# Kernel optimization log

Hardware: AMD Instinct MI355X
Metric: run time of the kernel (lower is better)

The kernel has to match this reference:

```python
import jax, jax.numpy as jnp
import numpy as np

NUM_HEADS = 8
NUM_LEVELS = 4
NUM_POINTS = 8
EMBED = 256
SPATIAL_SHAPES = ((92, 160), (46, 80), (23, 40), (12, 20))


def _bilinear_sample(vl, gx, gy, H, W):
    # vl: [N, d, H*W]; gx, gy: [N, Q, P], grid coords in [-1, 1]
    # matches F.grid_sample(mode='bilinear', padding_mode='zeros', align_corners=False)
    x = (gx + 1.0) * (W * 0.5) - 0.5
    y = (gy + 1.0) * (H * 0.5) - 0.5
    x0 = jnp.floor(x)
    y0 = jnp.floor(y)
    wx = x - x0
    wy = y - y0
    x0i = x0.astype(jnp.int32)
    y0i = y0.astype(jnp.int32)
    N, Q, P = gx.shape
    d = vl.shape[1]

    def gather(xi, yi):
        valid = ((xi >= 0) & (xi < W) & (yi >= 0) & (yi < H)).astype(vl.dtype)
        idx = jnp.clip(yi, 0, H - 1) * W + jnp.clip(xi, 0, W - 1)  # [N, Q, P]
        flat = jnp.broadcast_to(idx.reshape(N, 1, Q * P), (N, d, Q * P))
        got = jnp.take_along_axis(vl, flat, axis=2).reshape(N, d, Q, P)
        return got * valid[:, None]

    return (gather(x0i, y0i) * ((1 - wx) * (1 - wy))[:, None]
            + gather(x0i + 1, y0i) * (wx * (1 - wy))[:, None]
            + gather(x0i, y0i + 1) * ((1 - wx) * wy)[:, None]
            + gather(x0i + 1, y0i + 1) * (wx * wy)[:, None])


def _forward(query, value, reference_points, spatial_shapes,
             W_off, b_off, W_attn, b_attn, W_val, b_val, W_out, b_out):
    shapes = np.asarray(spatial_shapes)  # static per-level (H, W)
    bs, Q, C = query.shape
    H, Lv, P = NUM_HEADS, NUM_LEVELS, NUM_POINTS
    d = C // H
    # value projection, split into heads: [bs*H, d, Ltot]
    v = value @ W_val + b_val
    v = v.reshape(bs, -1, H, d).transpose(0, 2, 3, 1).reshape(bs * H, d, -1)
    # sampling offsets [bs, Q, H, Lv, P, 2]
    off = (query @ W_off + b_off).reshape(bs, Q, H, Lv, P, 2)
    # attention weights, softmax over Lv*P
    aw = jax.nn.softmax((query @ W_attn + b_attn).reshape(bs, Q, H, Lv * P), axis=-1)
    aw = aw.reshape(bs, Q, H, Lv, P).transpose(0, 2, 1, 3, 4).reshape(bs * H, Q, Lv, P)
    # normalize offsets by level (W, H)
    norm = jnp.asarray([[w_, h_] for h_, w_ in shapes], dtype=query.dtype)  # [Lv, 2]
    loc = reference_points[:, :, None, :, None, :] + off / norm[None, None, None, :, None, :]
    grids = (2.0 * loc - 1.0).transpose(0, 2, 1, 3, 4, 5).reshape(bs * H, Q, Lv, P, 2)
    out = jnp.zeros((bs * H, d, Q), dtype=query.dtype)
    start = 0
    for lvl in range(Lv):
        H_l, W_l = int(shapes[lvl, 0]), int(shapes[lvl, 1])
        vl = v[:, :, start:start + H_l * W_l]
        g = grids[:, :, lvl]  # [bs*H, Q, P, 2]
        s = _bilinear_sample(vl, g[..., 0], g[..., 1], H_l, W_l)  # [bs*H, d, Q, P]
        out = out + jnp.einsum('ndqp,nqp->ndq', s, aw[:, :, lvl])
        start += H_l * W_l
    out = out.reshape(bs, H, d, Q).transpose(0, 3, 1, 2).reshape(bs, Q, C)
    return out @ W_out + b_out


def setup_inputs() -> dict:
    key = jax.random.key(0)
    ks = jax.random.split(key, 9)
    bs, Q = 6, 4096  # 6 cameras x (64x64 BEV queries)
    Ltot = sum(h * w for h, w in SPATIAL_SHAPES)  # 19560
    HLP2 = NUM_HEADS * NUM_LEVELS * NUM_POINTS * 2  # 512
    HLP = NUM_HEADS * NUM_LEVELS * NUM_POINTS  # 256
    s = 0.02
    return {
        "query": jax.random.normal(ks[0], (bs, Q, EMBED), jnp.float32),
        "value": jax.random.normal(ks[1], (bs, Ltot, EMBED), jnp.float32),
        "reference_points": jax.random.uniform(ks[2], (bs, Q, NUM_LEVELS, 2), jnp.float32),
        "spatial_shapes": jnp.asarray(SPATIAL_SHAPES, jnp.int32),
        "W_off": s * jax.random.normal(ks[3], (EMBED, HLP2), jnp.float32),
        "b_off": s * jax.random.normal(ks[4], (HLP2,), jnp.float32),
        "W_attn": s * jax.random.normal(ks[5], (EMBED, HLP), jnp.float32),
        "b_attn": s * jax.random.normal(ks[6], (HLP,), jnp.float32),
        "W_val": s * jax.random.normal(ks[7], (EMBED, EMBED), jnp.float32),
        "b_val": jnp.zeros((EMBED,), jnp.float32),
        "W_out": s * jax.random.normal(ks[8], (EMBED, EMBED), jnp.float32),
        "b_out": jnp.zeros((EMBED,), jnp.float32),
    }


def reference(query, value, reference_points, spatial_shapes,
              W_off, b_off, W_attn, b_attn, W_val, b_val, W_out, b_out):
    return _forward(query, value, reference_points, spatial_shapes,
                    W_off, b_off, W_attn, b_attn, W_val, b_val, W_out, b_out)
```

## Files before the change

kernel.cpp:

```cpp
#include <hip/hip_runtime.h>
#include <hip/hip_fp16.h>
#include <stdint.h>

#define BS 6
#define NQ 4096
#define NH 8
#define EMB 256
#define LTOT 19560
#define ROWS_V 117360
#define ROWS_VP 117376
#define ROWS_Q 24576
#define VBLK 917
#define QBLK 1152

typedef __attribute__((ext_vector_type(8))) short bf16x8;
typedef __attribute__((ext_vector_type(4))) float floatx4;
typedef __attribute__((ext_vector_type(8))) unsigned short ushort8v;

__device__ __forceinline__ ushort f2bf(float f) {
    union { float f; uint32_t i; } c; c.f = f;
    uint32_t r = c.i + 0x7FFFu + ((c.i >> 16) & 1u);
    return (ushort)(r >> 16);
}
__device__ __forceinline__ ushort f2h(float f) {
    __half h = __float2half(f);
    union { __half h; ushort u; } c; c.h = h; return c.u;
}
__device__ __forceinline__ float h2f(ushort u) {
    union { ushort u; __half h; } c; c.u = u; return __half2float(c.h);
}

__device__ __forceinline__ void gll16(const ushort* g, ushort* l) {
    __builtin_amdgcn_global_load_lds(
        (const __attribute__((address_space(1))) void*)g,
        (__attribute__((address_space(3))) void*)l, 16, 0, 0);
}

template<int L>
__device__ __forceinline__ float bcastf(float x) {
    return __int_as_float(
        __builtin_amdgcn_ds_swizzle(__float_as_int(x), 0x1C | (L << 5)));
}
template<int L>
__device__ __forceinline__ uint32_t bcastu(uint32_t x) {
    return (uint32_t)__builtin_amdgcn_ds_swizzle((int)x, 0x1C | (L << 5));
}

__device__ __forceinline__ void fmx_lo(float& acc, float w, uint32_t u) {
    asm("v_fma_mix_f32 %0, %1, %2, %0 op_sel:[0,0,0] op_sel_hi:[0,1,0]"
        : "+v"(acc) : "v"(w), "v"(u));
}
__device__ __forceinline__ void fmx_hi(float& acc, float w, uint32_t u) {
    asm("v_fma_mix_f32 %0, %1, %2, %0 op_sel:[0,1,0] op_sel_hi:[0,1,0]"
        : "+v"(acc) : "v"(w), "v"(u));
}

__global__ __launch_bounds__(256) void prep(
    const float* __restrict__ W_val, const float* __restrict__ W_off,
    const float* __restrict__ W_attn, const float* __restrict__ W_out,
    const float* __restrict__ b_off, const float* __restrict__ b_attn,
    ushort* __restrict__ Wvt, ushort* __restrict__ Wq,
    ushort* __restrict__ Wot, float* __restrict__ bcat)
{
    int id = blockIdx.x * 256 + threadIdx.x;
    if (id < 65536) {
        int n = id >> 8, k = id & 255;
        Wvt[id] = f2bf(W_val[k * 256 + n]);
        return;
    }
    id -= 65536;
    if (id < 131072) {
        int n = id >> 8, k = id & 255;
        Wq[id] = f2bf(W_off[k * 512 + n]);
        return;
    }
    id -= 131072;
    if (id < 65536) {
        int n = id >> 8, k = id & 255;
        Wq[131072 + id] = f2bf(W_attn[k * 256 + n]);
        return;
    }
    id -= 65536;
    if (id < 65536) {
        int n = id >> 8, k = id & 255;
        Wot[id] = f2bf(W_out[k * 256 + n]);
        return;
    }
    id -= 65536;
    if (id < 768) bcat[id] = (id < 512) ? b_off[id] : b_attn[id - 512];
}

__global__ __launch_bounds__(512) void front(
    const float* __restrict__ value,
    const float* __restrict__ query,
    const ushort* __restrict__ Wvt,
    const ushort* __restrict__ Wq,
    const float* __restrict__ b_val,
    const float* __restrict__ bcat,
    ushort* __restrict__ v_out,
    ushort* __restrict__ qp_out)
{
    constexpr int K = 256;
    __shared__ ushort As[128 * 32];
    __shared__ ushort Bs[256 * 32];

    const int t = threadIdx.x;
    const int w = t >> 6;
    const int lane = t & 63;
    const int bid = blockIdx.x;

    if (bid < VBLK) {
        constexpr int N = 256, M = ROWS_V;
        const int bm = bid * 128;
        const int wm = (w >> 2) * 64;
        const int wn = (w & 3) * 64;

        const int arow = t >> 2;
        const int acol = (t & 3) * 8;
        const bool rowok = (bm + arow) < M;
        const float* Ap = value + (size_t)(bm + arow) * K + acol;
        ushort* Asw = &As[arow * 32 + acol];

        const int srow = lane >> 2;
        const int scol = (lane & 3) * 8;
        const ushort* Bg0 = Wvt + (size_t)(w * 32 + srow) * K + scol;
        const ushort* Bg1 = Wvt + (size_t)(w * 32 + 16 + srow) * K + scol;
        ushort* Bl0 = &Bs[(w * 32) * 32];
        ushort* Bl1 = &Bs[(w * 32 + 16) * 32];

        const ushort* apt = &As[(wm + (lane & 15)) * 32 + (lane >> 4) * 8];
        const ushort* bpt = &Bs[(wn + (lane & 15)) * 32 + (lane >> 4) * 8];

        floatx4 acc[4][4] = {};

        for (int kt = 0; kt < K; kt += 32) {
            float4 f0, f1;
            if (rowok) {
                f0 = *(const float4*)(Ap + kt);
                f1 = *(const float4*)(Ap + kt + 4);
            } else {
                f0 = make_float4(0.f, 0.f, 0.f, 0.f);
                f1 = f0;
            }
            __syncthreads();
            gll16(Bg0 + kt, Bl0);
            gll16(Bg1 + kt, Bl1);
            ushort8v u;
            u[0] = f2bf(f0.x); u[1] = f2bf(f0.y); u[2] = f2bf(f0.z); u[3] = f2bf(f0.w);
            u[4] = f2bf(f1.x); u[5] = f2bf(f1.y); u[6] = f2bf(f1.z); u[7] = f2bf(f1.w);
            *(ushort8v*)Asw = u;
            __syncthreads();

            bf16x8 a[4], b[4];
            #pragma unroll
            for (int i = 0; i < 4; ++i) {
                a[i] = *(const bf16x8*)(apt + i * 16 * 32);
                b[i] = *(const bf16x8*)(bpt + i * 16 * 32);
            }
            #pragma unroll
            for (int i = 0; i < 4; ++i)
                #pragma unroll
                for (int j = 0; j < 4; ++j)
                    acc[i][j] = __builtin_amdgcn_mfma_f32_16x16x32_bf16(
                        a[i], b[j], acc[i][j], 0, 0, 0);
        }

        const int crow = (lane >> 4) * 4;
        const int ccol = lane & 15;
        #pragma unroll
        for (int j = 0; j < 4; ++j) {
            int gcol = wn + j * 16 + ccol;
            float bv = b_val[gcol];
            #pragma unroll
            for (int i = 0; i < 4; ++i) {
                #pragma unroll
                for (int r = 0; r < 4; ++r) {
                    int grow = bm + wm + i * 16 + crow + r;
                    if (grow < M)
                        v_out[(size_t)grow * N + gcol] = f2h(acc[i][j][r] + bv);
                }
            }
        }
    } else {
        constexpr int N = 768;
        const int qbid = bid - VBLK;
        const int bm = (qbid % 192) * 128;
        const int bn = (qbid / 192) * 128;
        const int wm = (w >> 1) * 32;
        const int wn = (w & 1) * 64;

        const int arow = t >> 2;
        const int acol = (t & 3) * 8;
        const float* Ap = query + (size_t)(bm + arow) * K + acol;
        ushort* Asw = &As[arow * 32 + acol];

        const int srow = lane >> 2;
        const int scol = (lane & 3) * 8;
        const ushort* Bg0 = Wq + (size_t)(bn + w * 16 + srow) * K + scol;
        ushort* Bl0 = &Bs[(w * 16) * 32];

        const ushort* apt = &As[(wm + (lane & 15)) * 32 + (lane >> 4) * 8];
        const ushort* bpt = &Bs[(wn + (lane & 15)) * 32 + (lane >> 4) * 8];

        floatx4 acc[2][4] = {};

        for (int kt = 0; kt < K; kt += 32) {
            float4 f0 = *(const float4*)(Ap + kt);
            float4 f1 = *(const float4*)(Ap + kt + 4);
            __syncthreads();
            gll16(Bg0 + kt, Bl0);
            ushort8v u;
            u[0] = f2bf(f0.x); u[1] = f2bf(f0.y); u[2] = f2bf(f0.z); u[3] = f2bf(f0.w);
            u[4] = f2bf(f1.x); u[5] = f2bf(f1.y); u[6] = f2bf(f1.z); u[7] = f2bf(f1.w);
            *(ushort8v*)Asw = u;
            __syncthreads();

            bf16x8 a[2], b[4];
            #pragma unroll
            for (int i = 0; i < 2; ++i)
                a[i] = *(const bf16x8*)(apt + i * 16 * 32);
            #pragma unroll
            for (int j = 0; j < 4; ++j)
                b[j] = *(const bf16x8*)(bpt + j * 16 * 32);
            #pragma unroll
            for (int i = 0; i < 2; ++i)
                #pragma unroll
                for (int j = 0; j < 4; ++j)
                    acc[i][j] = __builtin_amdgcn_mfma_f32_16x16x32_bf16(
                        a[i], b[j], acc[i][j], 0, 0, 0);
        }

        const int crow = (lane >> 4) * 4;
        const int ccol = lane & 15;
        #pragma unroll
        for (int j = 0; j < 4; ++j) {
            int gcol = bn + wn + j * 16 + ccol;
            float bv = bcat[gcol];
            #pragma unroll
            for (int i = 0; i < 2; ++i) {
                int grow = bm + wm + i * 16 + crow;
                #pragma unroll
                for (int r = 0; r < 4; ++r)
                    qp_out[(size_t)(grow + r) * N + gcol] = f2h(acc[i][j][r] + bv);
            }
        }
    }
}

__global__ __launch_bounds__(256) void gemm_bt(
    const ushort* __restrict__ A,
    const ushort* __restrict__ Bt,
    const float* __restrict__ bias,
    float* __restrict__ C, int M, int N)
{
    constexpr int K = 256;
    __shared__ ushort As[128 * 32];
    __shared__ ushort Bs[128 * 32];

    const int t = threadIdx.x;
    const int w = t >> 6;
    const int lane = t & 63;
    const int bm = blockIdx.x * 128;
    const int bn = blockIdx.y * 128;
    const int wm = (w >> 1) * 64;
    const int wn = (w & 1) * 64;

    floatx4 acc[4][4] = {};

    const int srow = lane >> 2;
    const int scol = (lane & 3) * 8;
    const ushort* Ag0 = A + (size_t)(bm + (w * 2 + 0) * 16 + srow) * K + scol;
    const ushort* Ag1 = A + (size_t)(bm + (w * 2 + 1) * 16 + srow) * K + scol;
    const ushort* Bg0 = Bt + (size_t)(bn + (w * 2 + 0) * 16 + srow) * K + scol;
    const ushort* Bg1 = Bt + (size_t)(bn + (w * 2 + 1) * 16 + srow) * K + scol;
    ushort* Al0 = &As[(w * 2 + 0) * 512];
    ushort* Al1 = &As[(w * 2 + 1) * 512];
    ushort* Bl0 = &Bs[(w * 2 + 0) * 512];
    ushort* Bl1 = &Bs[(w * 2 + 1) * 512];

    const ushort* apt = &As[(wm + (lane & 15)) * 32 + (lane >> 4) * 8];
    const ushort* bpt = &Bs[(wn + (lane & 15)) * 32 + (lane >> 4) * 8];

    for (int kt = 0; kt < K; kt += 32) {
        __syncthreads();
        gll16(Ag0 + kt, Al0);
        gll16(Ag1 + kt, Al1);
        gll16(Bg0 + kt, Bl0);
        gll16(Bg1 + kt, Bl1);
        __syncthreads();

        bf16x8 a[4], b[4];
        #pragma unroll
        for (int i = 0; i < 4; ++i) {
            a[i] = *(const bf16x8*)(apt + i * 16 * 32);
            b[i] = *(const bf16x8*)(bpt + i * 16 * 32);
        }
        #pragma unroll
        for (int i = 0; i < 4; ++i)
            #pragma unroll
            for (int j = 0; j < 4; ++j)
                acc[i][j] = __builtin_amdgcn_mfma_f32_16x16x32_bf16(
                    a[i], b[j], acc[i][j], 0, 0, 0);
    }

    const int crow = (lane >> 4) * 4;
    const int ccol = lane & 15;
    #pragma unroll
    for (int j = 0; j < 4; ++j) {
        int gcol = bn + wn + j * 16 + ccol;
        float bv = bias[gcol];
        #pragma unroll
        for (int i = 0; i < 4; ++i) {
            #pragma unroll
            for (int r = 0; r < 4; ++r) {
                int grow = bm + wm + i * 16 + crow + r;
                if (grow < M)
                    C[(size_t)grow * N + gcol] = acc[i][j][r] + bv;
            }
        }
    }
}

__global__ __launch_bounds__(256) void sampler4(
    const ushort* __restrict__ v,
    const ushort* __restrict__ qp,
    const float* __restrict__ ref,
    ushort* __restrict__ agg)
{
    __shared__ char ballast[49152];
    if (blockIdx.x > 0x7FFFFFF0u) {
        ballast[threadIdx.x] = (char)threadIdx.x;
        agg[0] = (ushort)ballast[(threadIdx.x * 37) & 4095];
    }

    const int bid = (blockIdx.x & 7) * 384 + (blockIdx.x >> 3);

    const int tid = threadIdx.x;
    const int g = bid * 64 + (tid >> 2);
    const int st = tid & 3;
    const int h = g & 7;
    const int bq = g >> 3;
    const int b = bid >> 9;

    const int Wl = 160 >> st;
    const int Hl = (st == 3) ? 12 : (92 >> st);
    const int Sl = (st == 0) ? 0 : (st == 1) ? 14720 : (st == 2) ? 18400 : 19320;

    const ushort* qrow = qp + (size_t)bq * 768;

    float px[8], py[8];
    {
        ushort8v uo0 = *(const ushort8v*)(qrow + h * 64 + st * 16);
        ushort8v uo1 = *(const ushort8v*)(qrow + h * 64 + st * 16 + 8);
        float2 rf = *(const float2*)(ref + (size_t)bq * 8 + st * 2);
        const float fW = (float)Wl, fH = (float)Hl;
        #pragma unroll
        for (int i = 0; i < 4; ++i) {
            px[i]     = fmaf(rf.x, fW, h2f(uo0[2 * i]))     - 0.5f;
            py[i]     = fmaf(rf.y, fH, h2f(uo0[2 * i + 1])) - 0.5f;
            px[i + 4] = fmaf(rf.x, fW, h2f(uo1[2 * i]))     - 0.5f;
            py[i + 4] = fmaf(rf.y, fH, h2f(uo1[2 * i + 1])) - 0.5f;
        }
    }

    float a8[8];
    {
        ushort8v ul = *(const ushort8v*)(qrow + 512 + h * 32 + st * 8);
        #pragma unroll
        for (int i = 0; i < 8; ++i) a8[i] = h2f(ul[i]);
        float m = a8[0];
        #pragma unroll
        for (int i = 1; i < 8; ++i) m = fmaxf(m, a8[i]);
        m = fmaxf(m, __shfl_xor(m, 1, 4));
        m = fmaxf(m, __shfl_xor(m, 2, 4));
        float s = 0.f;
        #pragma unroll
        for (int i = 0; i < 8; ++i) { a8[i] = __expf(a8[i] - m); s += a8[i]; }
        s += __shfl_xor(s, 1, 4);
        s += __shfl_xor(s, 2, 4);
        float inv = 1.f / s;
        #pragma unroll
        for (int i = 0; i < 8; ++i) a8[i] *= inv;
    }

    const char* vb = (const char*)(v + (size_t)b * (LTOT * EMB));
    const uint32_t coffB = (uint32_t)(h * 64 + st * 16);

    float acc[8] = {0.f, 0.f, 0.f, 0.f, 0.f, 0.f, 0.f, 0.f};

    #pragma unroll
    for (int idx = 0; idx < 8; ++idx) {
        float px_ = px[idx], py_ = py[idx];
        float x0f = floorf(px_), y0f = floorf(py_);
        float wx = px_ - x0f, wy = py_ - y0f;
        int x0 = (int)x0f, y0 = (int)y0f;
        int x1 = x0 + 1, y1 = y0 + 1;
        float vx0 = ((uint32_t)x0 < (uint32_t)Wl) ? 1.f : 0.f;
        float vx1 = ((uint32_t)x1 < (uint32_t)Wl) ? 1.f : 0.f;
        float vy0 = ((uint32_t)y0 < (uint32_t)Hl) ? 1.f : 0.f;
        float vy1 = ((uint32_t)y1 < (uint32_t)Hl) ? 1.f : 0.f;
        int cx0 = min(max(x0, 0), Wl - 1);
        int cx1 = min(max(x1, 0), Wl - 1);
        int cy0 = min(max(y0, 0), Hl - 1);
        int cy1 = min(max(y1, 0), Hl - 1);
        float aw = a8[idx];
        float omx = 1.f - wx, omy = 1.f - wy;
        float omya = omy * aw, wya = wy * aw;
        float w00 = omx * omya * (vx0 * vy0);
        float w10 = wx  * omya * (vx1 * vy0);
        float w01 = omx * wya  * (vx0 * vy1);
        float w11 = wx  * wya  * (vx1 * vy1);
        int r0 = Sl + cy0 * Wl;
        int r1 = Sl + cy1 * Wl;
        uint32_t e00 = (uint32_t)(r0 + cx0) << 9;
        uint32_t e10 = (uint32_t)(r0 + cx1) << 9;
        uint32_t e01 = (uint32_t)(r1 + cx0) << 9;
        uint32_t e11 = (uint32_t)(r1 + cx1) << 9;

        #define ACCMIX(w_, c_) \
            fmx_lo(acc[0], w_, c_.x); fmx_hi(acc[1], w_, c_.x); \
            fmx_lo(acc[2], w_, c_.y); fmx_hi(acc[3], w_, c_.y); \
            fmx_lo(acc[4], w_, c_.z); fmx_hi(acc[5], w_, c_.z); \
            fmx_lo(acc[6], w_, c_.w); fmx_hi(acc[7], w_, c_.w);
        #define DO_LEVEL(L) { \
            float W00 = bcastf<L>(w00), W10 = bcastf<L>(w10); \
            float W01 = bcastf<L>(w01), W11 = bcastf<L>(w11); \
            uint32_t E00 = bcastu<L>(e00), E10 = bcastu<L>(e10); \
            uint32_t E01 = bcastu<L>(e01), E11 = bcastu<L>(e11); \
            uint4 c00 = *(const uint4*)(vb + (E00 + coffB)); \
            uint4 c10 = *(const uint4*)(vb + (E10 + coffB)); \
            uint4 c01 = *(const uint4*)(vb + (E01 + coffB)); \
            uint4 c11 = *(const uint4*)(vb + (E11 + coffB)); \
            ACCMIX(W00, c00); ACCMIX(W10, c10); \
            ACCMIX(W01, c01); ACCMIX(W11, c11); }
        DO_LEVEL(0)
        DO_LEVEL(1)
        DO_LEVEL(2)
        DO_LEVEL(3)
        #undef DO_LEVEL
        #undef ACCMIX
    }

    ushort8v r;
    #pragma unroll
    for (int i = 0; i < 8; ++i) r[i] = f2bf(acc[i]);
    *(ushort8v*)(agg + (size_t)bq * 256 + h * 32 + st * 8) = r;
}

extern "C" void kernel_launch(void* const* d_in, const int* in_sizes, int n_in,
                              void* d_out, int out_size, void* d_ws, size_t ws_size,
                              hipStream_t stream) {
    const float* query  = (const float*)d_in[0];
    const float* value  = (const float*)d_in[1];
    const float* refpts = (const float*)d_in[2];
    const float* W_off  = (const float*)d_in[4];
    const float* b_off  = (const float*)d_in[5];
    const float* W_attn = (const float*)d_in[6];
    const float* b_attn = (const float*)d_in[7];
    const float* W_val  = (const float*)d_in[8];
    const float* b_val  = (const float*)d_in[9];
    const float* W_out  = (const float*)d_in[10];
    const float* b_out  = (const float*)d_in[11];
    float* out = (float*)d_out;

    char* ws = (char*)d_ws;
    ushort* v_bf   = (ushort*)(ws);
    ushort* qp     = (ushort*)(ws + 72679424ull);
    ushort* agg_bf = (ushort*)(ws + 148176896ull);
    ushort* Wvt    = (ushort*)(ws + 160759808ull);
    ushort* Wq     = (ushort*)(ws + 160890880ull);
    ushort* Wot    = (ushort*)(ws + 161284096ull);
    float*  bcat   = (float*) (ws + 161415168ull);

    prep<<<1283, 256, 0, stream>>>(W_val, W_off, W_attn, W_out,
                                   b_off, b_attn, Wvt, Wq, Wot, bcat);

    front<<<VBLK + QBLK, 512, 0, stream>>>(
        value, query, Wvt, Wq, b_val, bcat, v_bf, qp);

    sampler4<<<(ROWS_Q * NH) / 64, 256, 0, stream>>>(
        v_bf, qp, refpts, agg_bf);

    gemm_bt<<<dim3(ROWS_Q / 128, 2), 256, 0, stream>>>(
        agg_bf, Wot, b_out, out, ROWS_Q, 256);
}
```

Before: 404.8 us.

## Restructure front GEMM: resident swizzled B tile in LDS, A streamed to registers

```diff
diff --git a/kernel.cpp b/kernel.cpp
--- a/kernel.cpp
+++ b/kernel.cpp
@@ -10,8 +10,8 @@
 #define ROWS_V 117360
 #define ROWS_VP 117376
 #define ROWS_Q 24576
-#define VBLK 917
-#define QBLK 1152
+#define VB2 1834
+#define QB 1152
 
 typedef __attribute__((ext_vector_type(8))) short bf16x8;
 typedef __attribute__((ext_vector_type(4))) float floatx4;
@@ -28,6 +28,11 @@
 }
 __device__ __forceinline__ float h2f(ushort u) {
     union { ushort u; __half h; } c; c.u = u; return __half2float(c.h);
+}
+__device__ __forceinline__ uint32_t cvtpk(float a, float b) {
+    uint32_t r;
+    asm("v_cvt_pk_bf16_f32 %0, %1, %2" : "=v"(r) : "v"(a), "v"(b));
+    return r;
 }
 
 __device__ __forceinline__ void gll16(const ushort* g, ushort* l) {
@@ -65,19 +70,19 @@
     int id = blockIdx.x * 256 + threadIdx.x;
     if (id < 65536) {
         int n = id >> 8, k = id & 255;
-        Wvt[id] = f2bf(W_val[k * 256 + n]);
+        Wvt[id ^ ((n & 7) << 3)] = f2bf(W_val[k * 256 + n]);
         return;
     }
     id -= 65536;
     if (id < 131072) {
         int n = id >> 8, k = id & 255;
-        Wq[id] = f2bf(W_off[k * 512 + n]);
+        Wq[id ^ ((n & 7) << 3)] = f2bf(W_off[k * 512 + n]);
         return;
     }
     id -= 131072;
     if (id < 65536) {
         int n = id >> 8, k = id & 255;
-        Wq[131072 + id] = f2bf(W_attn[k * 256 + n]);
+        Wq[131072 + (id ^ ((n & 7) << 3))] = f2bf(W_attn[k * 256 + n]);
         return;
     }
     id -= 65536;
@@ -90,7 +95,7 @@
     if (id < 768) bcat[id] = (id < 512) ? b_off[id] : b_attn[id - 512];
 }
 
-__global__ __launch_bounds__(512) void front(
+__global__ __launch_bounds__(512, 4) void front(
     const float* __restrict__ value,
     const float* __restrict__ query,
     const ushort* __restrict__ Wvt,
@@ -100,148 +105,101 @@
     ushort* __restrict__ v_out,
     ushort* __restrict__ qp_out)
 {
-    constexpr int K = 256;
-    __shared__ ushort As[128 * 32];
-    __shared__ ushort Bs[256 * 32];
+    __shared__ ushort Bs[128 * 256];
 
     const int t = threadIdx.x;
     const int w = t >> 6;
     const int lane = t & 63;
     const int bid = blockIdx.x;
 
-    if (bid < VBLK) {
-        constexpr int N = 256, M = ROWS_V;
-        const int bm = bid * 128;
-        const int wm = (w >> 2) * 64;
-        const int wn = (w & 3) * 64;
-
-        const int arow = t >> 2;
-        const int acol = (t & 3) * 8;
-        const bool rowok = (bm + arow) < M;
-        const float* Ap = value + (size_t)(bm + arow) * K + acol;
-        ushort* Asw = &As[arow * 32 + acol];
-
-        const int srow = lane >> 2;
-        const int scol = (lane & 3) * 8;
-        const ushort* Bg0 = Wvt + (size_t)(w * 32 + srow) * K + scol;
-        const ushort* Bg1 = Wvt + (size_t)(w * 32 + 16 + srow) * K + scol;
-        ushort* Bl0 = &Bs[(w * 32) * 32];
-        ushort* Bl1 = &Bs[(w * 32 + 16) * 32];
-
-        const ushort* apt = &As[(wm + (lane & 15)) * 32 + (lane >> 4) * 8];
-        const ushort* bpt = &Bs[(wn + (lane & 15)) * 32 + (lane >> 4) * 8];
-
-        floatx4 acc[4][4] = {};
-
-        for (int kt = 0; kt < K; kt += 32) {
+    const float* Ap;
+    const ushort* Bsrc;
+    const float* bias;
+    ushort* Cout;
+    int Nout, bm, bn, Mrows;
+    if (bid < VB2) {
+        int m = bid >> 1, nh = bid & 1;
+        bm = m * 128; bn = nh * 128;
+        Ap = value; Bsrc = Wvt + bn * 256; bias = b_val; Cout = v_out;
+        Nout = 256; Mrows = ROWS_V;
+    } else {
+        int qb = bid - VB2;
+        int m = qb / 6, nh = qb - m * 6;
+        bm = m * 128; bn = nh * 128;
+        Ap = query; Bsrc = Wq + bn * 256; bias = bcat; Cout = qp_out;
+        Nout = 768; Mrows = ROWS_Q;
+    }
+
+    #pragma unroll
+    for (int i = 0; i < 8; ++i)
+        gll16(Bsrc + i * 4096 + t * 8, &Bs[i * 4096 + t * 8]);
+    __syncthreads();
+
+    const int wm = (w >> 2) * 64;
+    const int wn = (w & 3) * 32;
+    const int ks = (lane >> 4) * 8;
+    const int arow0 = bm + wm + (lane & 15);
+
+    const int nl0 = wn + (lane & 15);
+    const int bsw = (nl0 & 7) << 3;
+    int bbase[2];
+    #pragma unroll
+    for (int j = 0; j < 2; ++j)
+        bbase[j] = (nl0 + j * 16) * 256 + ks;
+
+    const float* arow_p[4];
+    bool rok[4];
+    #pragma unroll
+    for (int i = 0; i < 4; ++i) {
+        int r = arow0 + i * 16;
+        rok[i] = r < Mrows;
+        arow_p[i] = Ap + (size_t)r * 256 + ks;
+    }
+
+    floatx4 acc[4][2] = {};
+
+    for (int kt = 0; kt < 256; kt += 32) {
+        bf16x8 a[4], b[2];
+        #pragma unroll
+        for (int i = 0; i < 4; ++i) {
             float4 f0, f1;
-            if (rowok) {
-                f0 = *(const float4*)(Ap + kt);
-                f1 = *(const float4*)(Ap + kt + 4);
+            if (rok[i]) {
+                f0 = *(const float4*)(arow_p[i] + kt);
+                f1 = *(const float4*)(arow_p[i] + kt + 4);
             } else {
-                f0 = make_float4(0.f, 0.f, 0.f, 0.f);
-                f1 = f0;
+                f0 = make_float4(0.f, 0.f, 0.f, 0.f); f1 = f0;
             }
-            __syncthreads();
-            gll16(Bg0 + kt, Bl0);
-            gll16(Bg1 + kt, Bl1);
-            ushort8v u;
-            u[0] = f2bf(f0.x); u[1] = f2bf(f0.y); u[2] = f2bf(f0.z); u[3] = f2bf(f0.w);
-            u[4] = f2bf(f1.x); u[5] = f2bf(f1.y); u[6] = f2bf(f1.z); u[7] = f2bf(f1.w);
-            *(ushort8v*)Asw = u;
-            __syncthreads();
-
-            bf16x8 a[4], b[4];
+            union { uint32_t u[4]; bf16x8 v; } cc;
+            cc.u[0] = cvtpk(f0.x, f0.y);
+            cc.u[1] = cvtpk(f0.z, f0.w);
+            cc.u[2] = cvtpk(f1.x, f1.y);
+            cc.u[3] = cvtpk(f1.z, f1.w);
+            a[i] = cc.v;
+        }
+        #pragma unroll
+        for (int j = 0; j < 2; ++j)
+            b[j] = *(const bf16x8*)&Bs[(bbase[j] + kt) ^ bsw];
+        #pragma unroll
+        for (int i = 0; i < 4; ++i)
             #pragma unroll
-            for (int i = 0; i < 4; ++i) {
-                a[i] = *(const bf16x8*)(apt + i * 16 * 32);
-                b[i] = *(const bf16x8*)(bpt + i * 16 * 32);
-            }
+            for (int j = 0; j < 2; ++j)
+                acc[i][j] = __builtin_amdgcn_mfma_f32_16x16x32_bf16(
+                    a[i], b[j], acc[i][j], 0, 0, 0);
+    }
+
+    const int crow = (lane >> 4) * 4;
+    const int ccol = lane & 15;
+    #pragma unroll
+    for (int j = 0; j < 2; ++j) {
+        int gcol = bn + wn + j * 16 + ccol;
+        float bv = bias[gcol];
+        #pragma unroll
+        for (int i = 0; i < 4; ++i) {
             #pragma unroll
-            for (int i = 0; i < 4; ++i)
-                #pragma unroll
-                for (int j = 0; j < 4; ++j)
-                    acc[i][j] = __builtin_amdgcn_mfma_f32_16x16x32_bf16(
-                        a[i], b[j], acc[i][j], 0, 0, 0);
-        }
-
-        const int crow = (lane >> 4) * 4;
-        const int ccol = lane & 15;
-        #pragma unroll
-        for (int j = 0; j < 4; ++j) {
-            int gcol = wn + j * 16 + ccol;
-            float bv = b_val[gcol];
-            #pragma unroll
-            for (int i = 0; i < 4; ++i) {
-                #pragma unroll
-                for (int r = 0; r < 4; ++r) {
-                    int grow = bm + wm + i * 16 + crow + r;
-                    if (grow < M)
-                        v_out[(size_t)grow * N + gcol] = f2h(acc[i][j][r] + bv);
-                }
-            }
-        }
-    } else {
-        constexpr int N = 768;
-        const int qbid = bid - VBLK;
-        const int bm = (qbid % 192) * 128;
-        const int bn = (qbid / 192) * 128;
-        const int wm = (w >> 1) * 32;
-        const int wn = (w & 1) * 64;
-
-        const int arow = t >> 2;
-        const int acol = (t & 3) * 8;
-        const float* Ap = query + (size_t)(bm + arow) * K + acol;
-        ushort* Asw = &As[arow * 32 + acol];
-
-        const int srow = lane >> 2;
-        const int scol = (lane & 3) * 8;
-        const ushort* Bg0 = Wq + (size_t)(bn + w * 16 + srow) * K + scol;
-        ushort* Bl0 = &Bs[(w * 16) * 32];
-
-        const ushort* apt = &As[(wm + (lane & 15)) * 32 + (lane >> 4) * 8];
-        const ushort* bpt = &Bs[(wn + (lane & 15)) * 32 + (lane >> 4) * 8];
-
-        floatx4 acc[2][4] = {};
-
-        for (int kt = 0; kt < K; kt += 32) {
-            float4 f0 = *(const float4*)(Ap + kt);
-            float4 f1 = *(const float4*)(Ap + kt + 4);
-            __syncthreads();
-            gll16(Bg0 + kt, Bl0);
-            ushort8v u;
-            u[0] = f2bf(f0.x); u[1] = f2bf(f0.y); u[2] = f2bf(f0.z); u[3] = f2bf(f0.w);
-            u[4] = f2bf(f1.x); u[5] = f2bf(f1.y); u[6] = f2bf(f1.z); u[7] = f2bf(f1.w);
-            *(ushort8v*)Asw = u;
-            __syncthreads();
-
-            bf16x8 a[2], b[4];
-            #pragma unroll
-            for (int i = 0; i < 2; ++i)
-                a[i] = *(const bf16x8*)(apt + i * 16 * 32);
-            #pragma unroll
-            for (int j = 0; j < 4; ++j)
-                b[j] = *(const bf16x8*)(bpt + j * 16 * 32);
-            #pragma unroll
-            for (int i = 0; i < 2; ++i)
-                #pragma unroll
-                for (int j = 0; j < 4; ++j)
-                    acc[i][j] = __builtin_amdgcn_mfma_f32_16x16x32_bf16(
-                        a[i], b[j], acc[i][j], 0, 0, 0);
-        }
-
-        const int crow = (lane >> 4) * 4;
-        const int ccol = lane & 15;
-        #pragma unroll
-        for (int j = 0; j < 4; ++j) {
-            int gcol = bn + wn + j * 16 + ccol;
-            float bv = bcat[gcol];
-            #pragma unroll
-            for (int i = 0; i < 2; ++i) {
-                int grow = bm + wm + i * 16 + crow;
-                #pragma unroll
-                for (int r = 0; r < 4; ++r)
-                    qp_out[(size_t)(grow + r) * N + gcol] = f2h(acc[i][j][r] + bv);
+            for (int r = 0; r < 4; ++r) {
+                int grow = bm + wm + i * 16 + crow + r;
+                if (grow < Mrows)
+                    Cout[(size_t)grow * Nout + gcol] = f2h(acc[i][j][r] + bv);
             }
         }
     }
@@ -475,7 +433,7 @@
     prep<<<1283, 256, 0, stream>>>(W_val, W_off, W_attn, W_out,
                                    b_off, b_attn, Wvt, Wq, Wot, bcat);
 
-    front<<<VBLK + QBLK, 512, 0, stream>>>(
+    front<<<VB2 + QB, 512, 0, stream>>>(
         value, query, Wvt, Wq, b_val, bcat, v_bf, qp);
 
     sampler4<<<(ROWS_Q * NH) / 64, 256, 0, stream>>>(
```

Result: slower. 495.7 us (+22.5%).
